# Kernel optimization log

Hardware: AMD Instinct MI355X
Metric: run time of the kernel (lower is better)

Reference implementation:

```python
import jax, jax.numpy as jnp
import numpy as np

MEAN_X = jnp.array([0.042766, 0.0081577, -0.015818, 9.2993, -0.087913, -3.3231], dtype=jnp.float32).reshape(6, 1)
STD_X = jnp.array([0.4142, 0.3522, 0.2881, 1.474, 0.6553, 0.8728], dtype=jnp.float32).reshape(6, 1)


def conv1d(x, w, b, pad, dil):
    # x: [B,C,L], w: [O,I,K] (torch OIH layout)
    y = jax.lax.conv_general_dilated(
        x, w, window_strides=(1,), padding=[(pad, pad)],
        rhs_dilation=(dil,), dimension_numbers=("NCH", "OIH", "NCH"))
    return y + b[None, :, None]


def setup_inputs() -> dict:
    key = jax.random.key(0)
    ks = jax.random.split(key, 20)
    f32 = jnp.float32
    return {
        "x": jax.random.normal(ks[0], (8192, 7, 200), dtype=f32),
        "calib_mat": 0.05 * jax.random.normal(ks[1], (6, 6), dtype=f32),
        "bias": 0.01 * jax.random.normal(ks[2], (6, 1), dtype=f32),
        "cw1": 0.1 * jax.random.normal(ks[3], (32, 6, 5), dtype=f32),
        "cb1": 0.01 * jax.random.normal(ks[4], (32,), dtype=f32),
        "cw2": 0.1 * jax.random.normal(ks[5], (32, 32, 5), dtype=f32),
        "cb2": 0.01 * jax.random.normal(ks[6], (32,), dtype=f32),
        "cw3": 0.1 * jax.random.normal(ks[7], (32, 32, 5), dtype=f32),
        "cb3": 0.01 * jax.random.normal(ks[8], (32,), dtype=f32),
        "cw4": 0.1 * jax.random.normal(ks[9], (1, 32, 5), dtype=f32),
        "cb4": 0.01 * jax.random.normal(ks[10], (1,), dtype=f32),
        "lw1": 0.05 * jax.random.normal(ks[11], (50, 192), dtype=f32),
        "lb1": 0.01 * jax.random.normal(ks[12], (50,), dtype=f32),
        "lw2": 0.05 * jax.random.normal(ks[13], (50, 50), dtype=f32),
        "lb2": 0.01 * jax.random.normal(ks[14], (50,), dtype=f32),
        "lw3": 0.05 * jax.random.normal(ks[15], (15, 50), dtype=f32),
        "lb3": 0.01 * jax.random.normal(ks[16], (15,), dtype=f32),
    }


def reference(x, calib_mat, bias, cw1, cb1, cw2, cb2, cw3, cb3, cw4, cb4,
              lw1, lb1, lw2, lb2, lw3, lb3):
    gelu = lambda t: jax.nn.gelu(t, approximate=False)  # torch default GELU is erf-based
    B = x.shape[0]
    imu = x[:, 1:, :]                                   # [B,6,L]
    M = jnp.eye(6, dtype=x.dtype) + calib_mat           # [6,6]
    xc = jnp.einsum("ij,bjl->bil", M, imu) + bias       # calibrate
    xn = (xc - MEAN_X) / STD_X                          # normalize
    h = gelu(conv1d(xn, cw1, cb1, pad=4, dil=1))        # [B,32,204]
    h = gelu(conv1d(h, cw2, cb2, pad=4, dil=3))         # [B,32,200]
    h = gelu(conv1d(h, cw3, cb3, pad=4, dil=3))         # [B,32,196]
    h = gelu(conv1d(h, cw4, cb4, pad=4, dil=3))         # [B,1,192]
    f = h.reshape(B, -1)                                # flatten -> [B,192]
    z = gelu(f @ lw1.T + lb1)
    z = gelu(z @ lw2.T + lb2)
    z = (z @ lw3.T + lb3) * 100.0                       # [B,15]
    R = z[:, :9].reshape(B, 3, 3)
    U, _, VT = jnp.linalg.svd(R, full_matrices=False)
    det = jnp.linalg.det(jnp.einsum("bij,bjk->bik", U, VT))  # sign of proper rotation
    scale = jnp.stack([jnp.ones_like(det), jnp.ones_like(det), det], axis=-1)  # diag(1,1,det)
    R_norm = jnp.einsum("bij,bjk->bik", U, VT * scale[:, :, None])
    return jnp.concatenate([R_norm.reshape(B, 9), z[:, 9:]], axis=1)
```

## Files before the change

kernel.cpp:

```cpp
#include <hip/hip_runtime.h>
#include <hip/hip_bf16.h>
#include <math.h>

#define NTHREADS 256
typedef __attribute__((ext_vector_type(8))) short short8;
typedef __attribute__((ext_vector_type(4))) float f32x4;
typedef unsigned short ushort_t;

#define HA    0
#define HB    8480
#define HSTR  40
#define SMEM_HW 16960

#define WSF_C1 0
#define WSF_C2 (10*512)
#define WSF_C3 (20*512)
#define WSF_C4 (30*512)
#define WS_F_BYTE_OFF 65536

__device__ __forceinline__ unsigned f2bf(float f) {
    unsigned u = __float_as_uint(f);
    return (u + 0x7FFFu + ((u >> 16) & 1u)) >> 16;
}

__device__ __forceinline__ unsigned pack2bf(float a, float b) {
    __hip_bfloat162 h = __float22bfloat162_rn(make_float2(a, b));
    unsigned u; __builtin_memcpy(&u, &h, 4); return u;
}

__device__ __forceinline__ float gelu_fast(float x) {
    float x2 = x * x;
    float t  = fmaf(0.10294320f, x2, 2.3022082f);
    float e  = __builtin_amdgcn_exp2f(x * t);
    float r  = __builtin_amdgcn_rcpf(e + 1.0f);
    return fmaf(-x, r, x);
}

__device__ __forceinline__ float gelu_exact(float v) {
    return 0.5f * v * (1.0f + erff(v * 0.70710678118654752f));
}

#define JROT(Spp, Sqq, Spq, Sxp, Sxq, Vp0, Vq0, Vp1, Vq1, Vp2, Vq2)          \
    if (fabsf(Spq) > 1e-18f) {                                               \
        float tau = (Sqq - Spp) / (2.0f * Spq);                              \
        float tj = copysignf(1.0f, tau) / (fabsf(tau) + sqrtf(1.0f + tau*tau)); \
        float cj = 1.0f / sqrtf(1.0f + tj*tj);                               \
        float sj = tj * cj;                                                  \
        Spp -= tj * Spq; Sqq += tj * Spq; Spq = 0.0f;                        \
        float tmp0 = Sxp; Sxp = cj*tmp0 - sj*Sxq; Sxq = sj*tmp0 + cj*Sxq;    \
        float tv;                                                            \
        tv = Vp0; Vp0 = cj*tv - sj*Vq0; Vq0 = sj*tv + cj*Vq0;                \
        tv = Vp1; Vp1 = cj*tv - sj*Vq1; Vq1 = sj*tv + cj*Vq1;                \
        tv = Vp2; Vp2 = cj*tv - sj*Vq2; Vq2 = sj*tv + cj*Vq2;                \
    }

__global__ void prep_kernel(const float* __restrict__ cw1,
                            const float* __restrict__ cw2,
                            const float* __restrict__ cw3,
                            const float* __restrict__ cw4,
                            ushort_t* __restrict__ ws)
{
    const int fid = blockIdx.x;
    const int l = threadIdx.x >> 3, j = threadIdx.x & 7;
    const int lo = l & 15, q = l >> 4;
    const int k = q * 8 + j;
    float v = 0.0f;
    if (fid < 10) {
        int tap = fid >> 1, Mt = fid & 1, c = Mt * 16 + lo;
        if (k < 6) v = cw1[(c * 6 + k) * 5 + tap];
    } else if (fid < 20) {
        int f = fid - 10, tap = f >> 1, Mt = f & 1, c = Mt * 16 + lo;
        v = cw2[(c * 32 + k) * 5 + tap];
    } else if (fid < 30) {
        int f = fid - 20, tap = f >> 1, Mt = f & 1, c = Mt * 16 + lo;
        v = cw3[(c * 32 + k) * 5 + tap];
    } else {
        int tap = fid - 30;
        if (lo == 0) v = cw4[k * 5 + tap];
    }
    ws[fid * 512 + l * 8 + j] = (ushort_t)f2bf(v);
}

template<int DIL, bool TWO, bool EDGEB>
__device__ __forceinline__ void conv_tiles(
    const ushort_t* __restrict__ src, ushort_t* __restrict__ dst,
    const short8 A[5][2], f32x4 b0, f32x4 b1, int Lout,
    int lo16, int quad, int t0)
{
    f32x4 acc00 = b0, acc01 = b1, acc10 = b0, acc11 = b1;
    const int n0a = t0 * 16, n0b = (t0 + 4) * 16;
    const ushort_t* pa = src + (n0a + lo16) * HSTR + quad * 8;
    const ushort_t* pb = src + (n0b + lo16) * HSTR + quad * 8;
    #pragma unroll
    for (int t = 0; t < 5; t++) {
        short8 Ba = *(const short8*)(pa + DIL * HSTR * t);
        acc00 = __builtin_amdgcn_mfma_f32_16x16x32_bf16(A[t][0], Ba, acc00, 0, 0, 0);
        acc01 = __builtin_amdgcn_mfma_f32_16x16x32_bf16(A[t][1], Ba, acc01, 0, 0, 0);
        if (TWO) {
            short8 Bb;
            if (EDGEB && DIL == 3) {
                int rb = min(n0b + lo16 + 3 * t, 211);
                Bb = *(const short8*)(src + rb * HSTR + quad * 8);
            } else {
                Bb = *(const short8*)(pb + DIL * HSTR * t);
            }
            acc10 = __builtin_amdgcn_mfma_f32_16x16x32_bf16(A[t][0], Bb, acc10, 0, 0, 0);
            acc11 = __builtin_amdgcn_mfma_f32_16x16x32_bf16(A[t][1], Bb, acc11, 0, 0, 0);
        }
    }
    {
        ushort_t* row = dst + (4 + n0a + lo16) * HSTR;
        *(uint2*)(row + quad * 4) = make_uint2(
            pack2bf(gelu_fast(acc00[0]), gelu_fast(acc00[1])),
            pack2bf(gelu_fast(acc00[2]), gelu_fast(acc00[3])));
        *(uint2*)(row + 16 + quad * 4) = make_uint2(
            pack2bf(gelu_fast(acc01[0]), gelu_fast(acc01[1])),
            pack2bf(gelu_fast(acc01[2]), gelu_fast(acc01[3])));
    }
    if (TWO) {
        const int n = n0b + lo16;
        ushort_t* row = dst + (4 + n) * HSTR;
        if (EDGEB) {
            unsigned p00 = 0, p01 = 0, p10 = 0, p11 = 0;
            if (n < Lout) {
                p00 = pack2bf(gelu_fast(acc10[0]), gelu_fast(acc10[1]));
                p01 = pack2bf(gelu_fast(acc10[2]), gelu_fast(acc10[3]));
                p10 = pack2bf(gelu_fast(acc11[0]), gelu_fast(acc11[1]));
                p11 = pack2bf(gelu_fast(acc11[2]), gelu_fast(acc11[3]));
            }
            *(uint2*)(row + quad * 4)      = make_uint2(p00, p01);
            *(uint2*)(row + 16 + quad * 4) = make_uint2(p10, p11);
        } else {
            *(uint2*)(row + quad * 4) = make_uint2(
                pack2bf(gelu_fast(acc10[0]), gelu_fast(acc10[1])),
                pack2bf(gelu_fast(acc10[2]), gelu_fast(acc10[3])));
            *(uint2*)(row + 16 + quad * 4) = make_uint2(
                pack2bf(gelu_fast(acc11[0]), gelu_fast(acc11[1])),
                pack2bf(gelu_fast(acc11[2]), gelu_fast(acc11[3])));
        }
    }
}

template<int DIL>
__device__ __forceinline__ void conv_mfma(
    const ushort_t* __restrict__ src, ushort_t* __restrict__ dst,
    const ushort_t* __restrict__ wsf, const float* __restrict__ bias,
    int Lout, int lane, int wave)
{
    const int lo16 = lane & 15, quad = lane >> 4;
    short8 A[5][2];
    #pragma unroll
    for (int t = 0; t < 5; t++) {
        A[t][0] = *(const short8*)(wsf + (t * 2 + 0) * 512 + lane * 8);
        A[t][1] = *(const short8*)(wsf + (t * 2 + 1) * 512 + lane * 8);
    }
    f32x4 b0, b1;
    #pragma unroll
    for (int r = 0; r < 4; r++) { b0[r] = bias[quad * 4 + r]; b1[r] = bias[16 + quad * 4 + r]; }
    conv_tiles<DIL, true, false>(src, dst, A, b0, b1, Lout, lo16, quad, wave);
    if (wave == 0) conv_tiles<DIL, true, true>(src, dst, A, b0, b1, Lout, lo16, quad, 8);
    else           conv_tiles<DIL, false, false>(src, dst, A, b0, b1, Lout, lo16, quad, wave + 8);
}

__global__ void __launch_bounds__(NTHREADS, 4)
rminet_conv_kernel(const float* __restrict__ x,
                   const float* __restrict__ calib,
                   const float* __restrict__ biasv,
                   const float* __restrict__ cb1, const float* __restrict__ cb2,
                   const float* __restrict__ cb3, const float* __restrict__ cb4,
                   const ushort_t* __restrict__ wsp,
                   float* __restrict__ F)
{
    __shared__ __align__(16) ushort_t smh[SMEM_HW];
    const int tid  = threadIdx.x;
    const int b    = blockIdx.x;
    const int lane = tid & 63;
    const int wave = __builtin_amdgcn_readfirstlane(tid >> 6);

    {
        uint4* p = (uint4*)smh;
        for (int i = tid; i < 1140; i += NTHREADS) {
            int idx = (i < 20) ? i : ((i < 80) ? 1000 + (i - 20) : 1060 + (i - 80));
            p[idx] = make_uint4(0u, 0u, 0u, 0u);
        }
    }
    __syncthreads();

    if (tid < 200) {
        const float* xc = x + (size_t)b * 1400 + 200 + tid;
        float v[6];
        #pragma unroll
        for (int ch = 0; ch < 6; ch++) v[ch] = xc[ch * 200];
        const float MEANS[6]  = {0.042766f, 0.0081577f, -0.015818f, 9.2993f, -0.087913f, -3.3231f};
        const float INVSTD[6] = {1.f/0.4142f, 1.f/0.3522f, 1.f/0.2881f, 1.f/1.474f, 1.f/0.6553f, 1.f/0.8728f};
        float xn[6];
        #pragma unroll
        for (int i = 0; i < 6; i++) {
            float acc = biasv[i];
            #pragma unroll
            for (int jj = 0; jj < 6; jj++) {
                float m = calib[i * 6 + jj] + ((i == jj) ? 1.0f : 0.0f);
                acc = fmaf(m, v[jj], acc);
            }
            xn[i] = (acc - MEANS[i]) * INVSTD[i];
        }
        ushort_t* row = smh + HB + (4 + tid) * HSTR;
        *(uint2*)row = make_uint2(pack2bf(xn[0], xn[1]), pack2bf(xn[2], xn[3]));
        *(unsigned*)(row + 4) = pack2bf(xn[4], xn[5]);
    }
    __syncthreads();

    conv_mfma<1>(smh + HB, smh + HA, wsp + WSF_C1, cb1, 204, lane, wave);
    __syncthreads();
    conv_mfma<3>(smh + HA, smh + HB, wsp + WSF_C2, cb2, 200, lane, wave);
    __syncthreads();
    conv_mfma<3>(smh + HB, smh + HA, wsp + WSF_C3, cb3, 196, lane, wave);
    if (tid < 20) ((uint4*)smh)[1000 + tid] = make_uint4(0u, 0u, 0u, 0u);
    __syncthreads();

    {
        const int lo16 = lane & 15, quad = lane >> 4;
        short8 A4[5];
        #pragma unroll
        for (int t = 0; t < 5; t++)
            A4[t] = *(const short8*)(wsp + WSF_C4 + t * 512 + lane * 8);
        f32x4 acc[3];
        #pragma unroll
        for (int u = 0; u < 3; u++) acc[u] = (f32x4){0.f, 0.f, 0.f, 0.f};
        const ushort_t* p4[3];
        #pragma unroll
        for (int u = 0; u < 3; u++)
            p4[u] = smh + HA + ((wave + 4 * u) * 16 + lo16) * HSTR + quad * 8;
        #pragma unroll
        for (int t = 0; t < 5; t++) {
            #pragma unroll
            for (int u = 0; u < 3; u++) {
                short8 B = *(const short8*)(p4[u] + 3 * HSTR * t);
                acc[u] = __builtin_amdgcn_mfma_f32_16x16x32_bf16(A4[t], B, acc[u], 0, 0, 0);
            }
        }
        if (quad == 0) {
            const float c4 = cb4[0];
            #pragma unroll
            for (int u = 0; u < 3; u++) {
                int n = (wave + 4 * u) * 16 + lo16;
                F[(size_t)b * 192 + n] = gelu_fast(acc[u][0] + c4);
            }
        }
    }
}

#define TLW1 0
#define TLW2 2400
#define TLW3 3050
#define TFQ  3245
#define TZ1F 16052
#define TZVF 16884
#define TSM_FLOATS 17156

__global__ void __launch_bounds__(256)
rminet_tail_kernel(const float* __restrict__ F,
                   const float* __restrict__ lw1, const float* __restrict__ lb1,
                   const float* __restrict__ lw2, const float* __restrict__ lb2,
                   const float* __restrict__ lw3, const float* __restrict__ lb3,
                   float* __restrict__ out)
{
    __shared__ __align__(16) float smf[TSM_FLOATS];
    float4* smq = (float4*)smf;
    const int tid  = threadIdx.x;
    const int lane = tid & 63;
    const int g    = __builtin_amdgcn_readfirstlane(tid >> 6);
    const int i0   = blockIdx.x * 16;
    const int ib   = g * 4;

    for (int idx = tid; idx < 2400; idx += 256) {
        int j4 = idx / 50, c = idx - j4 * 50;
        smq[TLW1 + idx] = *(const float4*)&lw1[c * 192 + 4 * j4];
    }
    for (int idx = tid; idx < 650; idx += 256) {
        int j4 = idx / 50, c = idx - j4 * 50;
        const float* wr = lw2 + c * 50 + 4 * j4;
        float4 w;
        w.x = wr[0]; w.y = wr[1];
        w.z = (4 * j4 + 2 < 50) ? wr[2] : 0.0f;
        w.w = (4 * j4 + 3 < 50) ? wr[3] : 0.0f;
        smq[TLW2 + idx] = w;
    }
    for (int idx = tid; idx < 195; idx += 256) {
        int j4 = idx / 15, c = idx - j4 * 15;
        const float* wr = lw3 + c * 50 + 4 * j4;
        float4 w;
        w.x = wr[0]; w.y = wr[1];
        w.z = (4 * j4 + 2 < 50) ? wr[2] : 0.0f;
        w.w = (4 * j4 + 3 < 50) ? wr[3] : 0.0f;
        smq[TLW3 + idx] = w;
    }
    {
        const float4* G4 = (const float4*)F + (size_t)i0 * 48;
        for (int idx = tid; idx < 768; idx += 256) smq[TFQ + idx] = G4[idx];
    }
    if (tid < 32) smf[TZ1F + (tid >> 1) * 52 + 50 + (tid & 1)] = 0.0f;
    __syncthreads();

    const int cc = min(lane, 49);

    {
        float a0, a1, a2, a3;
        a0 = a1 = a2 = a3 = lb1[cc];
        for (int j4 = 0; j4 < 48; j4++) {
            float4 w = smq[TLW1 + j4 * 50 + cc];
            float4 f0 = smq[TFQ + (ib + 0) * 48 + j4];
            float4 f1 = smq[TFQ + (ib + 1) * 48 + j4];
            float4 f2 = smq[TFQ + (ib + 2) * 48 + j4];
            float4 f3 = smq[TFQ + (ib + 3) * 48 + j4];
            a0 = fmaf(w.x, f0.x, fmaf(w.y, f0.y, fmaf(w.z, f0.z, fmaf(w.w, f0.w, a0))));
            a1 = fmaf(w.x, f1.x, fmaf(w.y, f1.y, fmaf(w.z, f1.z, fmaf(w.w, f1.w, a1))));
            a2 = fmaf(w.x, f2.x, fmaf(w.y, f2.y, fmaf(w.z, f2.z, fmaf(w.w, f2.w, a2))));
            a3 = fmaf(w.x, f3.x, fmaf(w.y, f3.y, fmaf(w.z, f3.z, fmaf(w.w, f3.w, a3))));
        }
        if (lane < 50) {
            smf[TZ1F + (ib + 0) * 52 + lane] = gelu_exact(a0);
            smf[TZ1F + (ib + 1) * 52 + lane] = gelu_exact(a1);
            smf[TZ1F + (ib + 2) * 52 + lane] = gelu_exact(a2);
            smf[TZ1F + (ib + 3) * 52 + lane] = gelu_exact(a3);
        }
    }

    {
        float a0, a1, a2, a3;
        a0 = a1 = a2 = a3 = lb2[cc];
        for (int j4 = 0; j4 < 13; j4++) {
            float4 w = smq[TLW2 + j4 * 50 + cc];
            float4 z0 = *(const float4*)&smf[TZ1F + (ib + 0) * 52 + 4 * j4];
            float4 z1 = *(const float4*)&smf[TZ1F + (ib + 1) * 52 + 4 * j4];
            float4 z2 = *(const float4*)&smf[TZ1F + (ib + 2) * 52 + 4 * j4];
            float4 z3 = *(const float4*)&smf[TZ1F + (ib + 3) * 52 + 4 * j4];
            a0 = fmaf(w.x, z0.x, fmaf(w.y, z0.y, fmaf(w.z, z0.z, fmaf(w.w, z0.w, a0))));
            a1 = fmaf(w.x, z1.x, fmaf(w.y, z1.y, fmaf(w.z, z1.z, fmaf(w.w, z1.w, a1))));
            a2 = fmaf(w.x, z2.x, fmaf(w.y, z2.y, fmaf(w.z, z2.z, fmaf(w.w, z2.w, a2))));
            a3 = fmaf(w.x, z3.x, fmaf(w.y, z3.y, fmaf(w.z, z3.z, fmaf(w.w, z3.w, a3))));
        }
        if (lane < 50) {
            smf[TZ1F + (ib + 0) * 52 + lane] = gelu_exact(a0);
            smf[TZ1F + (ib + 1) * 52 + lane] = gelu_exact(a1);
            smf[TZ1F + (ib + 2) * 52 + lane] = gelu_exact(a2);
            smf[TZ1F + (ib + 3) * 52 + lane] = gelu_exact(a3);
        }
    }

    {
        const int c3 = min(lane, 14);
        float a0, a1, a2, a3;
        a0 = a1 = a2 = a3 = lb3[c3];
        for (int j4 = 0; j4 < 13; j4++) {
            float4 w = smq[TLW3 + j4 * 15 + c3];
            float4 z0 = *(const float4*)&smf[TZ1F + (ib + 0) * 52 + 4 * j4];
            float4 z1 = *(const float4*)&smf[TZ1F + (ib + 1) * 52 + 4 * j4];
            float4 z2 = *(const float4*)&smf[TZ1F + (ib + 2) * 52 + 4 * j4];
            float4 z3 = *(const float4*)&smf[TZ1F + (ib + 3) * 52 + 4 * j4];
            a0 = fmaf(w.x, z0.x, fmaf(w.y, z0.y, fmaf(w.z, z0.z, fmaf(w.w, z0.w, a0))));
            a1 = fmaf(w.x, z1.x, fmaf(w.y, z1.y, fmaf(w.z, z1.z, fmaf(w.w, z1.w, a1))));
            a2 = fmaf(w.x, z2.x, fmaf(w.y, z2.y, fmaf(w.z, z2.z, fmaf(w.w, z2.w, a2))));
            a3 = fmaf(w.x, z3.x, fmaf(w.y, z3.y, fmaf(w.z, z3.z, fmaf(w.w, z3.w, a3))));
        }
        if (lane < 15) {
            smf[TZVF + (ib + 0) * 17 + lane] = a0 * 100.0f;
            smf[TZVF + (ib + 1) * 17 + lane] = a1 * 100.0f;
            smf[TZVF + (ib + 2) * 17 + lane] = a2 * 100.0f;
            smf[TZVF + (ib + 3) * 17 + lane] = a3 * 100.0f;
        }
    }
    __syncthreads();

    if (g == 0 && lane < 16) {
        const float* zv = &smf[TZVF + lane * 17];
        float* ob = out + (size_t)(i0 + lane) * 15;
        #pragma unroll
        for (int c = 9; c < 15; c++) ob[c] = zv[c];

        const float A00 = zv[0], A01 = zv[1], A02 = zv[2];
        const float A10 = zv[3], A11 = zv[4], A12 = zv[5];
        const float A20 = zv[6], A21 = zv[7], A22 = zv[8];
        float S00 = A00*A00 + A10*A10 + A20*A20;
        float S01 = A00*A01 + A10*A11 + A20*A21;
        float S02 = A00*A02 + A10*A12 + A20*A22;
        float S11 = A01*A01 + A11*A11 + A21*A21;
        float S12 = A01*A02 + A11*A12 + A21*A22;
        float S22 = A02*A02 + A12*A12 + A22*A22;
        float V00=1.f, V01=0.f, V02=0.f;
        float V10=0.f, V11=1.f, V12=0.f;
        float V20=0.f, V21=0.f, V22=1.f;
        #pragma unroll
        for (int sweep = 0; sweep < 8; sweep++) {
            JROT(S00, S11, S01, S02, S12, V00, V01, V10, V11, V20, V21)
            JROT(S00, S22, S02, S01, S12, V00, V02, V10, V12, V20, V22)
            JROT(S11, S22, S12, S01, S02, V01, V02, V11, V12, V21, V22)
        }
        float e0 = S00, e1 = S11, e2 = S22;
        float va0=V00, va1=V10, va2=V20;
        float vb0=V01, vb1=V11, vb2=V21;
        float vc0=V02, vc1=V12, vc2=V22;
        float sgn = 1.0f, tq;
        if (e0 < e1) { tq=e0;e0=e1;e1=tq; tq=va0;va0=vb0;vb0=tq; tq=va1;va1=vb1;vb1=tq; tq=va2;va2=vb2;vb2=tq; sgn=-sgn; }
        if (e1 < e2) { tq=e1;e1=e2;e2=tq; tq=vb0;vb0=vc0;vc0=tq; tq=vb1;vb1=vc1;vc1=tq; tq=vb2;vb2=vc2;vc2=tq; sgn=-sgn; }
        if (e0 < e1) { tq=e0;e0=e1;e1=tq; tq=va0;va0=vb0;vb0=tq; tq=va1;va1=vb1;vb1=tq; tq=va2;va2=vb2;vb2=tq; sgn=-sgn; }
        vc0 *= sgn; vc1 *= sgn; vc2 *= sgn;
        float u10 = A00*va0 + A01*va1 + A02*va2;
        float u11 = A10*va0 + A11*va1 + A12*va2;
        float u12 = A20*va0 + A21*va1 + A22*va2;
        float n1 = sqrtf(u10*u10 + u11*u11 + u12*u12);
        float rn1 = (n1 > 1e-20f) ? 1.0f / n1 : 0.0f;
        u10 *= rn1; u11 *= rn1; u12 *= rn1;
        float u20 = A00*vb0 + A01*vb1 + A02*vb2;
        float u21 = A10*vb0 + A11*vb1 + A12*vb2;
        float u22 = A20*vb0 + A21*vb1 + A22*vb2;
        float d12 = u20*u10 + u21*u11 + u22*u12;
        u20 -= d12*u10; u21 -= d12*u11; u22 -= d12*u12;
        float n2 = sqrtf(u20*u20 + u21*u21 + u22*u22);
        float rn2 = (n2 > 1e-20f) ? 1.0f / n2 : 0.0f;
        u20 *= rn2; u21 *= rn2; u22 *= rn2;
        float u30 = u11*u22 - u12*u21;
        float u31 = u12*u20 - u10*u22;
        float u32 = u10*u21 - u11*u20;
        ob[0] = u10*va0 + u20*vb0 + u30*vc0;
        ob[1] = u10*va1 + u20*vb1 + u30*vc1;
        ob[2] = u10*va2 + u20*vb2 + u30*vc2;
        ob[3] = u11*va0 + u21*vb0 + u31*vc0;
        ob[4] = u11*va1 + u21*vb1 + u31*vc1;
        ob[5] = u11*va2 + u21*vb2 + u31*vc2;
        ob[6] = u12*va0 + u22*vb0 + u32*vc0;
        ob[7] = u12*va1 + u22*vb1 + u32*vc1;
        ob[8] = u12*va2 + u22*vb2 + u32*vc2;
    }
}

extern "C" void kernel_launch(void* const* d_in, const int* in_sizes, int n_in,
                              void* d_out, int out_size, void* d_ws, size_t ws_size,
                              hipStream_t stream) {
    (void)n_in; (void)out_size; (void)ws_size;
    const float* x     = (const float*)d_in[0];
    const float* calib = (const float*)d_in[1];
    const float* biasv = (const float*)d_in[2];
    const float* cw1   = (const float*)d_in[3];
    const float* cb1   = (const float*)d_in[4];
    const float* cw2   = (const float*)d_in[5];
    const float* cb2   = (const float*)d_in[6];
    const float* cw3   = (const float*)d_in[7];
    const float* cb3   = (const float*)d_in[8];
    const float* cw4   = (const float*)d_in[9];
    const float* cb4   = (const float*)d_in[10];
    const float* lw1   = (const float*)d_in[11];
    const float* lb1   = (const float*)d_in[12];
    const float* lw2   = (const float*)d_in[13];
    const float* lb2   = (const float*)d_in[14];
    const float* lw3   = (const float*)d_in[15];
    const float* lb3   = (const float*)d_in[16];
    float* out = (float*)d_out;
    ushort_t* wsh = (ushort_t*)d_ws;
    float* Fb = (float*)((char*)d_ws + WS_F_BYTE_OFF);
    const int B = in_sizes[0] / 1400;

    hipLaunchKernelGGL(prep_kernel, dim3(35), dim3(512), 0, stream,
                       cw1, cw2, cw3, cw4, wsh);
    hipLaunchKernelGGL(rminet_conv_kernel, dim3(B), dim3(NTHREADS), 0, stream,
                       x, calib, biasv, cb1, cb2, cb3, cb4,
                       (const ushort_t*)wsh, Fb);
    hipLaunchKernelGGL(rminet_tail_kernel, dim3(B / 16), dim3(256), 0, stream,
                       (const float*)Fb, lw1, lb1, lw2, lb2, lw3, lb3, out);
}
```

Before: 213.6 us.

## Pack conv1 taps into one MFMA K dimension and store activations as 16-byte rows

Conv1 has only 6 input channels, so the 5 taps times 6 channels (30 values) are packed into a single K=32 MFMA operand. The input is written pre-shifted into a separate shared buffer, which cuts conv1 from 5 taps × 2 MFMAs per tile to 2 MFMAs. The weight K ordering for later layers is permuted so that each lane writes its gelu outputs as one 16-byte row store instead of two 8-byte stores. The cost is extra shared-memory writes (five copies of each input row) and a more complex weight permutation, which must stay consistent with the MFMA output layout.

```diff
diff --git a/kernel.cpp b/kernel.cpp
--- a/kernel.cpp
+++ b/kernel.cpp
@@ -10,12 +10,14 @@
 #define HA    0
 #define HB    8480
 #define HSTR  40
+#define XB    8640
+#define XSTR  32
 #define SMEM_HW 16960
 
 #define WSF_C1 0
-#define WSF_C2 (10*512)
-#define WSF_C3 (20*512)
-#define WSF_C4 (30*512)
+#define WSF_C2 (2*512)
+#define WSF_C3 (12*512)
+#define WSF_C4 (22*512)
 #define WS_F_BYTE_OFF 65536
 
 __device__ __forceinline__ unsigned f2bf(float f) {
@@ -64,24 +66,42 @@
     const int l = threadIdx.x >> 3, j = threadIdx.x & 7;
     const int lo = l & 15, q = l >> 4;
     const int k = q * 8 + j;
+    const int pk = ((k >> 2) & 1) * 16 + (k >> 3) * 4 + (k & 3);
     float v = 0.0f;
-    if (fid < 10) {
-        int tap = fid >> 1, Mt = fid & 1, c = Mt * 16 + lo;
-        if (k < 6) v = cw1[(c * 6 + k) * 5 + tap];
-    } else if (fid < 20) {
-        int f = fid - 10, tap = f >> 1, Mt = f & 1, c = Mt * 16 + lo;
-        v = cw2[(c * 32 + k) * 5 + tap];
-    } else if (fid < 30) {
-        int f = fid - 20, tap = f >> 1, Mt = f & 1, c = Mt * 16 + lo;
-        v = cw3[(c * 32 + k) * 5 + tap];
+    if (fid < 2) {
+        int m = fid * 16 + lo;
+        if (k < 30) { int t = k / 6, c = k - 6 * t; v = cw1[(m * 6 + c) * 5 + t]; }
+    } else if (fid < 12) {
+        int f = fid - 2, tap = f >> 1, Mt = f & 1, m = Mt * 16 + lo;
+        v = cw2[(m * 32 + pk) * 5 + tap];
+    } else if (fid < 22) {
+        int f = fid - 12, tap = f >> 1, Mt = f & 1, m = Mt * 16 + lo;
+        v = cw3[(m * 32 + pk) * 5 + tap];
     } else {
-        int tap = fid - 30;
-        if (lo == 0) v = cw4[k * 5 + tap];
+        int tap = fid - 22;
+        if (lo == 0) v = cw4[pk * 5 + tap];
     }
     ws[fid * 512 + l * 8 + j] = (ushort_t)f2bf(v);
 }
 
-template<int DIL, bool TWO, bool EDGEB>
+template<bool EDGE>
+__device__ __forceinline__ void store_tile(
+    ushort_t* __restrict__ dst, const f32x4 a0, const f32x4 a1,
+    int n, int Lout, int quad)
+{
+    ushort_t* row = dst + (4 + n) * HSTR + quad * 8;
+    if (EDGE && n >= Lout) {
+        *(uint4*)row = make_uint4(0u, 0u, 0u, 0u);
+    } else {
+        *(uint4*)row = make_uint4(
+            pack2bf(gelu_fast(a0[0]), gelu_fast(a0[1])),
+            pack2bf(gelu_fast(a0[2]), gelu_fast(a0[3])),
+            pack2bf(gelu_fast(a1[0]), gelu_fast(a1[1])),
+            pack2bf(gelu_fast(a1[2]), gelu_fast(a1[3])));
+    }
+}
+
+template<bool TWO, bool EDGEB>
 __device__ __forceinline__ void conv_tiles(
     const ushort_t* __restrict__ src, ushort_t* __restrict__ dst,
     const short8 A[5][2], f32x4 b0, f32x4 b1, int Lout,
@@ -93,55 +113,26 @@
     const ushort_t* pb = src + (n0b + lo16) * HSTR + quad * 8;
     #pragma unroll
     for (int t = 0; t < 5; t++) {
-        short8 Ba = *(const short8*)(pa + DIL * HSTR * t);
+        short8 Ba = *(const short8*)(pa + 3 * HSTR * t);
         acc00 = __builtin_amdgcn_mfma_f32_16x16x32_bf16(A[t][0], Ba, acc00, 0, 0, 0);
         acc01 = __builtin_amdgcn_mfma_f32_16x16x32_bf16(A[t][1], Ba, acc01, 0, 0, 0);
         if (TWO) {
             short8 Bb;
-            if (EDGEB && DIL == 3) {
+            if (EDGEB) {
                 int rb = min(n0b + lo16 + 3 * t, 211);
                 Bb = *(const short8*)(src + rb * HSTR + quad * 8);
             } else {
-                Bb = *(const short8*)(pb + DIL * HSTR * t);
+                Bb = *(const short8*)(pb + 3 * HSTR * t);
             }
             acc10 = __builtin_amdgcn_mfma_f32_16x16x32_bf16(A[t][0], Bb, acc10, 0, 0, 0);
             acc11 = __builtin_amdgcn_mfma_f32_16x16x32_bf16(A[t][1], Bb, acc11, 0, 0, 0);
         }
     }
-    {
-        ushort_t* row = dst + (4 + n0a + lo16) * HSTR;
-        *(uint2*)(row + quad * 4) = make_uint2(
-            pack2bf(gelu_fast(acc00[0]), gelu_fast(acc00[1])),
-            pack2bf(gelu_fast(acc00[2]), gelu_fast(acc00[3])));
-        *(uint2*)(row + 16 + quad * 4) = make_uint2(
-            pack2bf(gelu_fast(acc01[0]), gelu_fast(acc01[1])),
-            pack2bf(gelu_fast(acc01[2]), gelu_fast(acc01[3])));
-    }
-    if (TWO) {
-        const int n = n0b + lo16;
-        ushort_t* row = dst + (4 + n) * HSTR;
-        if (EDGEB) {
-            unsigned p00 = 0, p01 = 0, p10 = 0, p11 = 0;
-            if (n < Lout) {
-                p00 = pack2bf(gelu_fast(acc10[0]), gelu_fast(acc10[1]));
-                p01 = pack2bf(gelu_fast(acc10[2]), gelu_fast(acc10[3]));
-                p10 = pack2bf(gelu_fast(acc11[0]), gelu_fast(acc11[1]));
-                p11 = pack2bf(gelu_fast(acc11[2]), gelu_fast(acc11[3]));
-            }
-            *(uint2*)(row + quad * 4)      = make_uint2(p00, p01);
-            *(uint2*)(row + 16 + quad * 4) = make_uint2(p10, p11);
-        } else {
-            *(uint2*)(row + quad * 4) = make_uint2(
-                pack2bf(gelu_fast(acc10[0]), gelu_fast(acc10[1])),
-                pack2bf(gelu_fast(acc10[2]), gelu_fast(acc10[3])));
-            *(uint2*)(row + 16 + quad * 4) = make_uint2(
-                pack2bf(gelu_fast(acc11[0]), gelu_fast(acc11[1])),
-                pack2bf(gelu_fast(acc11[2]), gelu_fast(acc11[3])));
-        }
-    }
-}
-
-template<int DIL>
+    store_tile<false>(dst, acc00, acc01, n0a + lo16, Lout, quad);
+    if (TWO) store_tile<EDGEB>(dst, acc10, acc11, n0b + lo16, Lout, quad);
+}
+
+template<int LAYER>
 __device__ __forceinline__ void conv_mfma(
     const ushort_t* __restrict__ src, ushort_t* __restrict__ dst,
     const ushort_t* __restrict__ wsf, const float* __restrict__ bias,
@@ -157,9 +148,40 @@
     f32x4 b0, b1;
     #pragma unroll
     for (int r = 0; r < 4; r++) { b0[r] = bias[quad * 4 + r]; b1[r] = bias[16 + quad * 4 + r]; }
-    conv_tiles<DIL, true, false>(src, dst, A, b0, b1, Lout, lo16, quad, wave);
-    if (wave == 0) conv_tiles<DIL, true, true>(src, dst, A, b0, b1, Lout, lo16, quad, 8);
-    else           conv_tiles<DIL, false, false>(src, dst, A, b0, b1, Lout, lo16, quad, wave + 8);
+    conv_tiles<true, false>(src, dst, A, b0, b1, Lout, lo16, quad, wave);
+    if (wave == 0) conv_tiles<true, true>(src, dst, A, b0, b1, Lout, lo16, quad, 8);
+    else           conv_tiles<false, false>(src, dst, A, b0, b1, Lout, lo16, quad, wave + 8);
+}
+
+__device__ __forceinline__ void conv1_packed(
+    const ushort_t* __restrict__ xb, ushort_t* __restrict__ dst,
+    const ushort_t* __restrict__ wsf, const float* __restrict__ bias,
+    int lane, int wave)
+{
+    const int lo16 = lane & 15, quad = lane >> 4;
+    const short8 A0 = *(const short8*)(wsf + 0 * 512 + lane * 8);
+    const short8 A1 = *(const short8*)(wsf + 1 * 512 + lane * 8);
+    f32x4 b0, b1;
+    #pragma unroll
+    for (int r = 0; r < 4; r++) { b0[r] = bias[quad * 4 + r]; b1[r] = bias[16 + quad * 4 + r]; }
+    f32x4 a0[3], a1[3];
+    #pragma unroll
+    for (int u = 0; u < 3; u++) {
+        const int n = (wave + 4 * u) * 16 + lo16;
+        short8 B = *(const short8*)(xb + n * XSTR + quad * 8);
+        a0[u] = __builtin_amdgcn_mfma_f32_16x16x32_bf16(A0, B, b0, 0, 0, 0);
+        a1[u] = __builtin_amdgcn_mfma_f32_16x16x32_bf16(A1, B, b1, 0, 0, 0);
+    }
+    #pragma unroll
+    for (int u = 0; u < 3; u++)
+        store_tile<false>(dst, a0[u], a1[u], (wave + 4 * u) * 16 + lo16, 204, quad);
+    if (wave == 0) {
+        const int n = 192 + lo16;
+        short8 B = *(const short8*)(xb + n * XSTR + quad * 8);
+        f32x4 e0 = __builtin_amdgcn_mfma_f32_16x16x32_bf16(A0, B, b0, 0, 0, 0);
+        f32x4 e1 = __builtin_amdgcn_mfma_f32_16x16x32_bf16(A1, B, b1, 0, 0, 0);
+        store_tile<true>(dst, e0, e1, n, 204, quad);
+    }
 }
 
 __global__ void __launch_bounds__(NTHREADS, 4)
@@ -179,8 +201,11 @@
 
     {
         uint4* p = (uint4*)smh;
-        for (int i = tid; i < 1140; i += NTHREADS) {
-            int idx = (i < 20) ? i : ((i < 80) ? 1000 + (i - 20) : 1060 + (i - 80));
+        for (int i = tid; i < 988; i += NTHREADS) {
+            int idx = (i < 20) ? i
+                    : (i < 80) ? 1000 + (i - 20)
+                    : (i < 948) ? 1060 + (i - 80)
+                    : 2080 + (i - 948);
             p[idx] = make_uint4(0u, 0u, 0u, 0u);
         }
     }
@@ -204,15 +229,24 @@
             }
             xn[i] = (acc - MEANS[i]) * INVSTD[i];
         }
-        ushort_t* row = smh + HB + (4 + tid) * HSTR;
-        *(uint2*)row = make_uint2(pack2bf(xn[0], xn[1]), pack2bf(xn[2], xn[3]));
-        *(unsigned*)(row + 4) = pack2bf(xn[4], xn[5]);
-    }
-    __syncthreads();
-
-    conv_mfma<1>(smh + HB, smh + HA, wsp + WSF_C1, cb1, 204, lane, wave);
-    __syncthreads();
-    conv_mfma<3>(smh + HA, smh + HB, wsp + WSF_C2, cb2, 200, lane, wave);
+        const unsigned d0 = pack2bf(xn[0], xn[1]);
+        const unsigned d1 = pack2bf(xn[2], xn[3]);
+        const unsigned d2 = pack2bf(xn[4], xn[5]);
+        const int trot = tid & 3;
+        #pragma unroll
+        for (int tt = 0; tt < 5; tt++) {
+            int t = tt + trot; if (t >= 5) t -= 5;
+            ushort_t* qp = smh + XB + (tid + 4 - t) * XSTR + t * 6;
+            *(unsigned*)(qp + 0) = d0;
+            *(unsigned*)(qp + 2) = d1;
+            *(unsigned*)(qp + 4) = d2;
+        }
+    }
+    __syncthreads();
+
+    conv1_packed(smh + XB, smh + HA, wsp + WSF_C1, cb1, lane, wave);
+    __syncthreads();
+    conv_mfma<2>(smh + HA, smh + HB, wsp + WSF_C2, cb2, 200, lane, wave);
     __syncthreads();
     conv_mfma<3>(smh + HB, smh + HA, wsp + WSF_C3, cb3, 196, lane, wave);
     if (tid < 20) ((uint4*)smh)[1000 + tid] = make_uint4(0u, 0u, 0u, 0u);
@@ -460,7 +494,7 @@
     float* Fb = (float*)((char*)d_ws + WS_F_BYTE_OFF);
     const int B = in_sizes[0] / 1400;
 
-    hipLaunchKernelGGL(prep_kernel, dim3(35), dim3(512), 0, stream,
+    hipLaunchKernelGGL(prep_kernel, dim3(27), dim3(512), 0, stream,
                        cw1, cw2, cw3, cw4, wsh);
     hipLaunchKernelGGL(rminet_conv_kernel, dim3(B), dim3(NTHREADS), 0, stream,
                        x, calib, biasv, cb1, cb2, cb3, cb4,
```

Result: faster. 206.4 us (-3.4%).
